# Optimization experiments

Hardware: AMD Instinct MI355X
Metric: run time of the kernel (lower is better)

The kernel has to match this reference:

```python
import jax, jax.numpy as jnp
import numpy as np

EMBED = 768
GH = 4        # heads per group
GD = 256      # group dim = GH * head_dim
NSTEPS = 3    # n_pde_steps
DT = 0.05
HJ_H = 0.05   # Heimburg-Jackson dispersion coefficient


def _sh(u, k):
    # shift field content along sequence axis (axis=1) by k with zero boundary
    if k == 0:
        return u
    z = jnp.zeros_like(u)
    if k > 0:
        return z.at[:, k:, :].set(u[:, :-k, :])
    return z.at[:, :k, :].set(u[:, -k:, :])


def _d1(u):
    return 0.5 * (_sh(u, -1) - _sh(u, 1))


def _d2(u):
    return _sh(u, -1) - 2.0 * u + _sh(u, 1)


def _d3(u):
    return 0.5 * (_sh(u, -2) - 2.0 * _sh(u, -1) + 2.0 * _sh(u, 1) - _sh(u, 2))


def _d4(u):
    return _sh(u, -2) - 4.0 * _sh(u, -1) + 6.0 * u - 4.0 * _sh(u, 1) + _sh(u, 2)


def _attn(x, qkv_w, qkv_b, ow, ob, nh):
    # standard causal multi-head attention on one head group
    B, T, D = x.shape
    hd = D // nh
    qkv = x @ qkv_w + qkv_b                      # (B,T,3D)
    q, k, v = jnp.split(qkv, 3, axis=-1)
    heads = lambda a: a.reshape(B, T, nh, hd).transpose(0, 2, 1, 3)
    q, k, v = heads(q), heads(k), heads(v)
    s = jnp.einsum('bhqd,bhkd->bhqk', q, k) * (1.0 / np.sqrt(hd))
    causal = jnp.tril(jnp.ones((T, T), dtype=bool))
    s = jnp.where(causal, s, jnp.asarray(-1e9, s.dtype))
    p = jax.nn.softmax(s, axis=-1)
    o = jnp.einsum('bhqk,bhkd->bhqd', p, v).transpose(0, 2, 1, 3).reshape(B, T, D)
    return o @ ow + ob


def _sine_gordon(u):
    # u_tt = u_xx - sin(u), semi-implicit Euler (leapfrog-like)
    w = jnp.zeros_like(u)
    for _ in range(NSTEPS):
        w = w + DT * (_d2(u) - jnp.sin(u))
        u = u + DT * w
    return u


def _kdv(u):
    # u_t = -6 u u_x - u_xxx, explicit Euler
    for _ in range(NSTEPS):
        u = u + DT * (-6.0 * u * _d1(u) - _d3(u))
    return u


def _hj(u):
    # Heimburg-Jackson: u_tt = d_xx((c0^2 + p u + q u^2) u) - h u_xxxx
    # with c0=1, p=-1, q=1
    w = jnp.zeros_like(u)
    for _ in range(NSTEPS):
        f = u - u * u + u * u * u
        w = w + DT * (_d2(f) - HJ_H * _d4(u))
        u = u + DT * w
    return u


def setup_inputs() -> dict:
    key = jax.random.key(0)
    ks = jax.random.split(key, 16)
    s = 0.02
    d, gd = EMBED, GD
    inp = {'x': jax.random.normal(ks[0], (4, 2048, d), dtype=jnp.float32)}
    inp['in_w'] = jax.random.normal(ks[1], (d, d), jnp.float32) * s
    inp['in_b'] = jnp.zeros((d,), jnp.float32)
    for i, n in enumerate(['sg', 'kdv', 'hj']):
        inp[n + '_qkv_w'] = jax.random.normal(ks[2 + 4 * i], (gd, 3 * gd), jnp.float32) * s
        inp[n + '_qkv_b'] = jnp.zeros((3 * gd,), jnp.float32)
        inp[n + '_out_w'] = jax.random.normal(ks[3 + 4 * i], (gd, gd), jnp.float32) * s
        inp[n + '_out_b'] = jnp.zeros((gd,), jnp.float32)
    inp['out_w'] = jax.random.normal(ks[14], (d, d), jnp.float32) * s
    inp['out_b'] = jnp.zeros((d,), jnp.float32)
    return inp


def reference(x, in_w, in_b,
              sg_qkv_w, sg_qkv_b, sg_out_w, sg_out_b,
              kdv_qkv_w, kdv_qkv_b, kdv_out_w, kdv_out_b,
              hj_qkv_w, hj_qkv_b, hj_out_w, hj_out_b,
              out_w, out_b):
    h = x @ in_w + in_b
    xg = jnp.split(h, [GD, 2 * GD], axis=-1)
    sg = _sine_gordon(_attn(xg[0], sg_qkv_w, sg_qkv_b, sg_out_w, sg_out_b, GH))
    kv = _kdv(_attn(xg[1], kdv_qkv_w, kdv_qkv_b, kdv_out_w, kdv_out_b, GH))
    hj = _hj(_attn(xg[2], hj_qkv_w, hj_qkv_b, hj_out_w, hj_out_b, GH))
    out = jnp.concatenate([sg, kv, hj], axis=-1)
    return out @ out_w + out_b
```

## Files before the change

### kernel.cpp

```cpp
#include <hip/hip_runtime.h>
#include <math.h>

#define B_   4
#define T_   2048
#define D_   768
#define M_   8192
#define GD_  256
#define NH_  4
#define HD_  64

typedef short  s16x8 __attribute__((ext_vector_type(8)));
typedef __bf16 bfx8  __attribute__((ext_vector_type(8)));
typedef float  fx4   __attribute__((ext_vector_type(4)));

#define LOG2E 1.44269504088896f
#define QSCALE (0.125f * LOG2E)

__device__ __forceinline__ short f2bf(float f) {
  union { float f; unsigned u; } v; v.f = f;
  unsigned r = v.u + 0x7fffu + ((v.u >> 16) & 1u);
  return (short)(r >> 16);
}

__device__ __forceinline__ unsigned cvt_pk_bf16(float lo, float hi) {
  unsigned r;
  asm("v_cvt_pk_bf16_f32 %0, %1, %2" : "=v"(r) : "v"(lo), "v"(hi));
  return r;
}

struct PW { const short* p0; const short* p1; const short* p2; };
struct PB { const float* p0; const float* p1; const float* p2; };
__device__ __forceinline__ const short* selw(const PW& s, int z) {
  return z == 0 ? s.p0 : (z == 1 ? s.p1 : s.p2);
}
__device__ __forceinline__ const float* selb(const PB& s, int z) {
  return z == 0 ? s.p0 : (z == 1 ? s.p1 : s.p2);
}

template<int AT, int OBF, int MODE>
__global__ __launch_bounds__(256) void gemm_mfma(
    const void* __restrict__ Avoid, long sA, int lda,
    PW Wp, PB Bp, int K,
    void* __restrict__ C, long sC, int ldc,
    void* __restrict__ xtra)
{
  __shared__ short As[128 * 72];
  __shared__ short Bs[64 * 72];

  const int z = blockIdx.z;
  const short* Ab16 = (const short*)Avoid + (long)z * sA;
  const float* Ab32 = (const float*)Avoid + (long)z * sA;
  const short* Wb = selw(Wp, z);
  const float* bb = selb(Bp, z);

  const int n0 = blockIdx.x * 64;
  const int m0 = blockIdx.y * 128;
  const int tid = threadIdx.x, lane = tid & 63, w = tid >> 6;
  const int wm = w >> 1, wn = w & 1;
  const int quad = lane >> 4, mr = lane & 15;

  const int r0 = tid >> 3;
  const int cs = (tid & 7) * 8;

  fx4 acc[4][2] = {};
  s16x8 ar[4], br[2];

  auto loadA = [&](int k0) {
#pragma unroll
    for (int gg = 0; gg < 4; ++gg) {
      if (AT) {
        const float* p = Ab32 + (long)(m0 + r0 + 32 * gg) * lda + k0 + cs;
        float4 f0 = *(const float4*)p;
        float4 f1 = *(const float4*)(p + 4);
        short o[8] = { f2bf(f0.x), f2bf(f0.y), f2bf(f0.z), f2bf(f0.w),
                       f2bf(f1.x), f2bf(f1.y), f2bf(f1.z), f2bf(f1.w) };
        ar[gg] = *(s16x8*)o;
      } else {
        ar[gg] = *(const s16x8*)(Ab16 + (long)(m0 + r0 + 32 * gg) * lda + k0 + cs);
      }
    }
  };
  auto loadB = [&](int k0) {
#pragma unroll
    for (int hh = 0; hh < 2; ++hh)
      br[hh] = *(const s16x8*)(Wb + (long)(n0 + r0 + 32 * hh) * K + k0 + cs);
  };

  loadA(0); loadB(0);

  for (int k0 = 0; k0 < K; k0 += 64) {
#pragma unroll
    for (int gg = 0; gg < 4; ++gg)
      *(s16x8*)&As[(r0 + 32 * gg) * 72 + cs] = ar[gg];
#pragma unroll
    for (int hh = 0; hh < 2; ++hh)
      *(s16x8*)&Bs[(r0 + 32 * hh) * 72 + cs] = br[hh];
    __syncthreads();

    if (k0 + 64 < K) { loadA(k0 + 64); loadB(k0 + 64); }

#pragma unroll
    for (int ks = 0; ks < 2; ++ks) {
      bfx8 af[4], bf[2];
#pragma unroll
      for (int i = 0; i < 4; ++i)
        af[i] = *(const bfx8*)&As[(wm * 64 + i * 16 + mr) * 72 + ks * 32 + quad * 8];
#pragma unroll
      for (int j = 0; j < 2; ++j)
        bf[j] = *(const bfx8*)&Bs[(wn * 32 + j * 16 + mr) * 72 + ks * 32 + quad * 8];
#pragma unroll
      for (int i = 0; i < 4; ++i)
#pragma unroll
        for (int j = 0; j < 2; ++j)
          acc[i][j] = __builtin_amdgcn_mfma_f32_16x16x32_bf16(af[i], bf[j], acc[i][j], 0, 0, 0);
    }
    __syncthreads();
  }

  float* Cf = (float*)C + (long)z * sC;
  short* Cs = (short*)C + (long)z * sC;
#pragma unroll
  for (int j = 0; j < 2; ++j) {
    const int col = n0 + wn * 32 + j * 16 + mr;
    const float bvx = bb[col];
#pragma unroll
    for (int i = 0; i < 4; ++i) {
      const int row0 = m0 + wm * 64 + i * 16 + quad * 4;
      if (MODE == 2) {
        const int rb = row0 >> 11, t0 = row0 & 2047;
        fx4 o;
#pragma unroll
        for (int r = 0; r < 4; ++r) o[r] = acc[i][j][r] + bvx;
        *(fx4*)((float*)xtra + (((long)z * B_ + rb) * GD_ + col) * T_ + t0) = o;
      } else if (MODE == 1 && col >= 512) {
        const int h = (col - 512) >> 6, hd = (col - 512) & 63;
        const int rb = row0 >> 11, t0 = row0 & 2047;
        short o4[4];
#pragma unroll
        for (int r = 0; r < 4; ++r) o4[r] = f2bf(acc[i][j][r] + bvx);
        *(short4*)((short*)xtra + ((((long)z * B_ + rb) * NH_ + h) * HD_ + hd) * T_ + t0) =
            *(short4*)o4;
      } else {
        const float sc = (MODE == 1 && col < 256) ? QSCALE : 1.0f;
#pragma unroll
        for (int r = 0; r < 4; ++r) {
          float v = (acc[i][j][r] + bvx) * sc;
          if (OBF) Cs[(long)(row0 + r) * ldc + col] = f2bf(v);
          else     Cf[(long)(row0 + r) * ldc + col] = v;
        }
      }
    }
  }
}

__global__ __launch_bounds__(256) void flash_attn_mfma(
    short* __restrict__ qkv, const short* __restrict__ vtb)
{
  __shared__ short Ks[64][72];
  __shared__ short Vs[80][72];
  __shared__ short Ps[128 * 64];

  const int bid = blockIdx.x;
  const int Q = 15 - (bid / 48);
  const int combo = bid % 48;
  const int g = combo % 3, bh = combo / 3;
  const int b = bh >> 2, h = bh & 3;

  short* base = qkv + ((size_t)g * M_ + (size_t)b * T_) * D_;
  short*       Qp = base + h * HD_;
  const short* Kp = base + GD_ + h * HD_;
  const short* Vtp = vtb + ((((size_t)g * B_ + b) * NH_ + h) * HD_) * T_;

  const int tid = threadIdx.x, lane = tid & 63, w = tid >> 6;
  const int quad = lane >> 4, mr = lane & 15;
  const int q0 = Q * 128, wr = w * 32;
  const int qhi = q0 + wr + 31;

  const int sra = tid >> 3, sc = (tid & 7) * 8;

  if (tid < 128) {
    const short ov = 0x3F80;
    s16x8 one = { ov, ov, ov, ov, ov, ov, ov, ov };
    *(s16x8*)&Vs[64 + (tid >> 3)][(tid & 7) * 8] = one;
  }

  bfx8 aq[2][2];
#pragma unroll
  for (int f = 0; f < 2; ++f)
#pragma unroll
    for (int ks = 0; ks < 2; ++ks)
      aq[f][ks] = *(const bfx8*)(Qp + (size_t)(q0 + wr + f * 16 + mr) * D_ +
                                 ks * 32 + quad * 8);

  s16x8 kreg0 = *(const s16x8*)(Kp + (size_t)sra * D_ + sc);
  s16x8 kreg1 = *(const s16x8*)(Kp + (size_t)(sra + 32) * D_ + sc);
  s16x8 vreg0 = *(const s16x8*)(Vtp + (size_t)sra * T_ + sc);
  s16x8 vreg1 = *(const s16x8*)(Vtp + (size_t)(sra + 32) * T_ + sc);

  fx4 Oa[2][5] = {};

  char* PsB = (char*)&Ps[0];
  const int rot = (mr & 7) << 4;

  const int ktmax = 2 * Q + 1;
  for (int kt = 0; kt <= ktmax; ++kt) {
    *(s16x8*)&Ks[sra][sc]      = kreg0;
    *(s16x8*)&Ks[sra + 32][sc] = kreg1;
    *(s16x8*)&Vs[sra][sc]      = vreg0;
    *(s16x8*)&Vs[sra + 32][sc] = vreg1;
    __syncthreads();

    if (kt < ktmax) {
      const int kn = (kt + 1) * 64;
      kreg0 = *(const s16x8*)(Kp + (size_t)(kn + sra) * D_ + sc);
      kreg1 = *(const s16x8*)(Kp + (size_t)(kn + sra + 32) * D_ + sc);
      vreg0 = *(const s16x8*)(Vtp + (size_t)sra * T_ + kn + sc);
      vreg1 = *(const s16x8*)(Vtp + (size_t)(sra + 32) * T_ + kn + sc);
    }

    if (kt * 64 <= qhi) {
      fx4 st[4][2] = {};
#pragma unroll
      for (int ks = 0; ks < 2; ++ks) {
        bfx8 bk[4];
#pragma unroll
        for (int jj = 0; jj < 4; ++jj)
          bk[jj] = *(const bfx8*)&Ks[jj * 16 + mr][ks * 32 + quad * 8];
#pragma unroll
        for (int jj = 0; jj < 4; ++jj)
#pragma unroll
          for (int f = 0; f < 2; ++f)
            st[jj][f] = __builtin_amdgcn_mfma_f32_16x16x32_bf16(bk[jj], aq[f][ks], st[jj][f], 0, 0, 0);
      }

      if (kt >= 2 * Q) {
#pragma unroll
        for (int jj = 0; jj < 4; ++jj)
#pragma unroll
          for (int f = 0; f < 2; ++f) {
            const int qg = q0 + wr + f * 16 + mr;
            const int kvg0 = kt * 64 + jj * 16 + quad * 4;
#pragma unroll
            for (int r = 0; r < 4; ++r)
              if (kvg0 + r > qg) st[jj][f][r] = -1e30f;
          }
      }

#pragma unroll
      for (int f = 0; f < 2; ++f) {
        const int rowb = (wr + f * 16 + mr) << 7;
#pragma unroll
        for (int jj = 0; jj < 4; ++jj) {
          float e0 = exp2f(st[jj][f][0]);
          float e1 = exp2f(st[jj][f][1]);
          float e2 = exp2f(st[jj][f][2]);
          float e3 = exp2f(st[jj][f][3]);
          unsigned pk0 = cvt_pk_bf16(e0, e1);
          unsigned pk1 = cvt_pk_bf16(e2, e3);
          unsigned long long pv = (unsigned long long)pk0 |
                                  ((unsigned long long)pk1 << 32);
          const int kb = (jj * 32 + quad * 8) ^ rot;
          *(unsigned long long*)(PsB + rowb + kb) = pv;
        }
      }

#pragma unroll
      for (int ks = 0; ks < 2; ++ks) {
        bfx8 ap[2];
#pragma unroll
        for (int f = 0; f < 2; ++f) {
          const int rowb = (wr + f * 16 + mr) << 7;
          const int kb = (ks * 64 + quad * 16) ^ rot;
          ap[f] = *(const bfx8*)(PsB + rowb + kb);
        }
#pragma unroll
        for (int j = 0; j < 5; ++j) {
          bfx8 bv = *(const bfx8*)&Vs[j * 16 + mr][ks * 32 + quad * 8];
#pragma unroll
          for (int f = 0; f < 2; ++f)
            Oa[f][j] = __builtin_amdgcn_mfma_f32_16x16x32_bf16(ap[f], bv, Oa[f][j], 0, 0, 0);
        }
      }
    }
    __syncthreads();
  }

#pragma unroll
  for (int f = 0; f < 2; ++f)
#pragma unroll
    for (int r = 0; r < 4; ++r) {
      const float inv = 1.0f / Oa[f][4][r];
      const int row = q0 + wr + f * 16 + quad * 4 + r;
#pragma unroll
      for (int j = 0; j < 4; ++j)
        Qp[(size_t)row * D_ + j * 16 + mr] = f2bf(Oa[f][j][r] * inv);
    }
}

__device__ __forceinline__ float fhj(float x) { return x - x * x + x * x * x; }

__global__ __launch_bounds__(256) void pde_kernel(
    const float* __restrict__ ut, short* __restrict__ ub)
{
  __shared__ short ob[4][2056];

  const int cg = blockIdx.x, b = blockIdx.y, g = blockIdx.z;
  const int tid = threadIdx.x;
  const int c = tid >> 6, lane = tid & 63;
  const int t0 = lane * 32;
  const float dt = 0.05f;

  const float* src = ut + (((size_t)g * B_ + b) * GD_ + cg * 4 + c) * T_ + t0;

  float uc[36];
#pragma unroll
  for (int q = 0; q < 8; ++q)
    *(fx4*)&uc[2 + q * 4] = *(const fx4*)(src + q * 4);

  {
    float h0 = __shfl_up(uc[32], 1);
    float h1 = __shfl_up(uc[33], 1);
    float h2 = __shfl_down(uc[2], 1);
    float h3 = __shfl_down(uc[3], 1);
    uc[0]  = (lane == 0)  ? 0.f : h0;
    uc[1]  = (lane == 0)  ? 0.f : h1;
    uc[34] = (lane == 63) ? 0.f : h2;
    uc[35] = (lane == 63) ? 0.f : h3;
  }

  float wreg[32];
#pragma unroll
  for (int i = 0; i < 32; ++i) wreg[i] = 0.f;

  for (int step = 0; step < 3; ++step) {
    float nu[32];
#pragma unroll
    for (int tt = 0; tt < 32; ++tt) {
      float um2 = uc[tt], um1 = uc[tt + 1], u = uc[tt + 2];
      float up1 = uc[tt + 3], up2 = uc[tt + 4];
      if (g == 0) {
        float d2 = up1 - 2.f * u + um1;
        wreg[tt] += dt * (d2 - __sinf(u));
        nu[tt] = u + dt * wreg[tt];
      } else if (g == 1) {
        float d1 = 0.5f * (up1 - um1);
        float d3 = 0.5f * (up2 - 2.f * up1 + 2.f * um1 - um2);
        nu[tt] = u + dt * (-6.f * u * d1 - d3);
      } else {
        float d2f = fhj(up1) - 2.f * fhj(u) + fhj(um1);
        float d4  = up2 - 4.f * up1 + 6.f * u - 4.f * um1 + um2;
        wreg[tt] += dt * (d2f - 0.05f * d4);
        nu[tt] = u + dt * wreg[tt];
      }
    }
    float h0 = __shfl_up(nu[30], 1);
    float h1 = __shfl_up(nu[31], 1);
    float h2 = __shfl_down(nu[0], 1);
    float h3 = __shfl_down(nu[1], 1);
    uc[0]  = (lane == 0)  ? 0.f : h0;
    uc[1]  = (lane == 0)  ? 0.f : h1;
    uc[34] = (lane == 63) ? 0.f : h2;
    uc[35] = (lane == 63) ? 0.f : h3;
#pragma unroll
    for (int i = 0; i < 32; ++i) uc[2 + i] = nu[i];
  }

  short o16[32];
#pragma unroll
  for (int i = 0; i < 32; ++i) o16[i] = f2bf(uc[2 + i]);
#pragma unroll
  for (int q = 0; q < 4; ++q)
    *(s16x8*)&ob[c][t0 + q * 8] = *(s16x8*)&o16[q * 8];
  __syncthreads();

  short* dst = ub + (size_t)b * T_ * D_ + g * GD_ + cg * 4;
#pragma unroll
  for (int q = 0; q < 8; ++q) {
    int t = tid + q * 256;
    short o4[4];
#pragma unroll
    for (int cc = 0; cc < 4; ++cc) o4[cc] = ob[cc][t];
    *(short4*)(dst + (size_t)t * D_) = *(short4*)o4;
  }
}

struct PrepArgs {
  const float* w[8]; short* wt[8];
  int K[8], N[8];
  int tend[8];
};

__global__ __launch_bounds__(256) void prep_kernel(PrepArgs pa)
{
  const int bid = blockIdx.x, tid = threadIdx.x;
  __shared__ float Ws[32][33];
  int ti = 0;
#pragma unroll
  for (int i = 0; i < 8; ++i) if (bid >= pa.tend[i]) ti = i + 1;
  const int tloc = bid - (ti ? pa.tend[ti - 1] : 0);
  const int K = pa.K[ti], N = pa.N[ti];
  const int ntx = N >> 5;
  const int k0 = (tloc / ntx) * 32, n0 = (tloc % ntx) * 32;
  const float* W = pa.w[ti];
  short* WT = pa.wt[ti];
  const int tx = tid & 31, ty = tid >> 5;

#pragma unroll
  for (int i = 0; i < 4; ++i)
    Ws[ty + 8 * i][tx] = W[(long)(k0 + ty + 8 * i) * N + n0 + tx];
  __syncthreads();
#pragma unroll
  for (int i = 0; i < 4; ++i) {
    int r = ty + 8 * i;
    WT[(long)(n0 + r) * K + k0 + tx] = f2bf(Ws[tx][r]);
  }
}

extern "C" void kernel_launch(void* const* d_in, const int* in_sizes, int n_in,
                              void* d_out, int out_size, void* d_ws, size_t ws_size,
                              hipStream_t stream)
{
  (void)in_sizes; (void)n_in; (void)out_size; (void)ws_size;

  const float* x         = (const float*)d_in[0];
  const float* in_w      = (const float*)d_in[1];
  const float* in_b      = (const float*)d_in[2];
  const float* sg_qkv_w  = (const float*)d_in[3];
  const float* sg_qkv_b  = (const float*)d_in[4];
  const float* sg_out_w  = (const float*)d_in[5];
  const float* sg_out_b  = (const float*)d_in[6];
  const float* kdv_qkv_w = (const float*)d_in[7];
  const float* kdv_qkv_b = (const float*)d_in[8];
  const float* kdv_out_w = (const float*)d_in[9];
  const float* kdv_out_b = (const float*)d_in[10];
  const float* hj_qkv_w  = (const float*)d_in[11];
  const float* hj_qkv_b  = (const float*)d_in[12];
  const float* hj_out_w  = (const float*)d_in[13];
  const float* hj_out_b  = (const float*)d_in[14];
  const float* out_w     = (const float*)d_in[15];
  const float* out_b     = (const float*)d_in[16];
  float* out = (float*)d_out;

  const size_t MD = (size_t)M_ * D_;
  short* base = (short*)d_ws;
  short* hb   = base + MD;
  float* uf   = (float*)d_ws;
  short* qkvb = base + 2 * MD;
  short* ub16 = qkvb + 3 * MD;
  short* wts  = ub16 + MD;
  short* in_wT  = wts;
  short* qkvT0  = in_wT + 589824;
  short* qkvT1  = qkvT0 + 196608;
  short* qkvT2  = qkvT1 + 196608;
  short* outT0  = qkvT2 + 196608;
  short* outT1  = outT0 + 65536;
  short* outT2  = outT1 + 65536;
  short* out_wT = outT2 + 65536;
  short* vtb    = out_wT + 589824;

  dim3 blk(256);

  PrepArgs pa;
  const float* wsrc[8] = { in_w, sg_qkv_w, kdv_qkv_w, hj_qkv_w,
                           sg_out_w, kdv_out_w, hj_out_w, out_w };
  short* wdst[8] = { in_wT, qkvT0, qkvT1, qkvT2, outT0, outT1, outT2, out_wT };
  int Ksz[8] = { 768, 256, 256, 256, 256, 256, 256, 768 };
  int Nsz[8] = { 768, 768, 768, 768, 256, 256, 256, 768 };
  int cum = 0;
  for (int i = 0; i < 8; ++i) {
    pa.w[i] = wsrc[i]; pa.wt[i] = wdst[i]; pa.K[i] = Ksz[i]; pa.N[i] = Nsz[i];
    cum += (Ksz[i] >> 5) * (Nsz[i] >> 5);
    pa.tend[i] = cum;
  }
  prep_kernel<<<dim3((unsigned)cum), blk, 0, stream>>>(pa);

  gemm_mfma<1, 1, 0><<<dim3(12, 64, 1), blk, 0, stream>>>(
      x, 0, D_, PW{in_wT, in_wT, in_wT}, PB{in_b, in_b, in_b}, D_,
      hb, 0, D_, nullptr);

  gemm_mfma<0, 1, 1><<<dim3(12, 64, 3), blk, 0, stream>>>(
      hb, 256, D_,
      PW{qkvT0, qkvT1, qkvT2}, PB{sg_qkv_b, kdv_qkv_b, hj_qkv_b}, GD_,
      qkvb, (long)MD, D_, vtb);

  flash_attn_mfma<<<dim3(768), blk, 0, stream>>>(qkvb, vtb);

  gemm_mfma<0, 0, 2><<<dim3(4, 64, 3), blk, 0, stream>>>(
      qkvb, (long)MD, D_,
      PW{outT0, outT1, outT2}, PB{sg_out_b, kdv_out_b, hj_out_b}, GD_,
      uf, 0, 0, uf);

  pde_kernel<<<dim3(64, 4, 3), blk, 0, stream>>>(uf, ub16);

  gemm_mfma<0, 0, 0><<<dim3(12, 64, 1), blk, 0, stream>>>(
      ub16, 0, D_, PW{out_wT, out_wT, out_wT}, PB{out_b, out_b, out_b}, D_,
      out, 0, D_, nullptr);
}
```

Baseline: 305.9 us.

## Use direct global-to-LDS loads with double buffering and XOR swizzle in GEMM

For the bf16-input GEMM path, register-staged loads are replaced with global_load_lds 16-byte direct-to-LDS transfers into double-buffered shared tiles. A waitcnt/barrier pipeline overlaps the next tile's fetch with MFMA compute on the current one. Padded LDS rows are replaced by an XOR swizzle to avoid bank conflicts, and the fp32-input path also adopts the swizzle. This aims to cut register staging and LDS write latency, but relies on correct vmcnt accounting and doubles the LDS footprint.

New measurement: 307.5 us. Within noise of the previous version (+0.5%).

```diff
diff --git a/kernel.cpp b/kernel.cpp
--- a/kernel.cpp
+++ b/kernel.cpp
@@ -28,6 +28,12 @@
   return r;
 }
 
+__device__ __forceinline__ void gload16(const void* g, void* l) {
+  __builtin_amdgcn_global_load_lds(
+      (const __attribute__((address_space(1))) unsigned int*)g,
+      (__attribute__((address_space(3))) unsigned int*)l, 16, 0, 0);
+}
+
 struct PW { const short* p0; const short* p1; const short* p2; };
 struct PB { const float* p0; const float* p1; const float* p2; };
 __device__ __forceinline__ const short* selw(const PW& s, int z) {
@@ -44,8 +50,8 @@
     void* __restrict__ C, long sC, int ldc,
     void* __restrict__ xtra)
 {
-  __shared__ short As[128 * 72];
-  __shared__ short Bs[64 * 72];
+  __shared__ short As[2][128 * 64];
+  __shared__ short Bs[2][64 * 64];
 
   const int z = blockIdx.z;
   const short* Ab16 = (const short*)Avoid + (long)z * sA;
@@ -59,62 +65,101 @@
   const int wm = w >> 1, wn = w & 1;
   const int quad = lane >> 4, mr = lane & 15;
 
-  const int r0 = tid >> 3;
-  const int cs = (tid & 7) * 8;
-
   fx4 acc[4][2] = {};
-  s16x8 ar[4], br[2];
-
-  auto loadA = [&](int k0) {
-#pragma unroll
-    for (int gg = 0; gg < 4; ++gg) {
-      if (AT) {
+
+  auto compute = [&](const short* Ab, const short* Bb) {
+#pragma unroll
+    for (int ks = 0; ks < 2; ++ks) {
+      const int cc = ks * 32 + quad * 8;
+      const int swz = cc ^ ((mr & 7) * 8);
+      bfx8 af[4], bf[2];
+#pragma unroll
+      for (int i = 0; i < 4; ++i)
+        af[i] = *(const bfx8*)&Ab[(wm * 64 + i * 16 + mr) * 64 + swz];
+#pragma unroll
+      for (int j = 0; j < 2; ++j)
+        bf[j] = *(const bfx8*)&Bb[(wn * 32 + j * 16 + mr) * 64 + swz];
+#pragma unroll
+      for (int i = 0; i < 4; ++i)
+#pragma unroll
+        for (int j = 0; j < 2; ++j)
+          acc[i][j] = __builtin_amdgcn_mfma_f32_16x16x32_bf16(af[i], bf[j], acc[i][j], 0, 0, 0);
+    }
+  };
+
+  if (AT) {
+    const int r0 = tid >> 3;
+    const int cs = (tid & 7) * 8;
+    const int wswz = cs ^ ((r0 & 7) * 8);
+    s16x8 ar[4], br[2];
+
+    auto loadA = [&](int k0) {
+#pragma unroll
+      for (int gg = 0; gg < 4; ++gg) {
         const float* p = Ab32 + (long)(m0 + r0 + 32 * gg) * lda + k0 + cs;
         float4 f0 = *(const float4*)p;
         float4 f1 = *(const float4*)(p + 4);
         short o[8] = { f2bf(f0.x), f2bf(f0.y), f2bf(f0.z), f2bf(f0.w),
                        f2bf(f1.x), f2bf(f1.y), f2bf(f1.z), f2bf(f1.w) };
         ar[gg] = *(s16x8*)o;
+      }
+    };
+    auto loadB = [&](int k0) {
+#pragma unroll
+      for (int hh = 0; hh < 2; ++hh)
+        br[hh] = *(const s16x8*)(Wb + (long)(n0 + r0 + 32 * hh) * K + k0 + cs);
+    };
+
+    loadA(0); loadB(0);
+    for (int k0 = 0; k0 < K; k0 += 64) {
+#pragma unroll
+      for (int gg = 0; gg < 4; ++gg)
+        *(s16x8*)&As[0][(r0 + 32 * gg) * 64 + wswz] = ar[gg];
+#pragma unroll
+      for (int hh = 0; hh < 2; ++hh)
+        *(s16x8*)&Bs[0][(r0 + 32 * hh) * 64 + wswz] = br[hh];
+      __syncthreads();
+      if (k0 + 64 < K) { loadA(k0 + 64); loadB(k0 + 64); }
+      compute(&As[0][0], &Bs[0][0]);
+      __syncthreads();
+    }
+  } else {
+    const int lrow = lane >> 3, lcol = lane & 7;
+
+    auto stageA = [&](short* dst, int k0) {
+#pragma unroll
+      for (int i = 0; i < 4; ++i) {
+        const int r = i * 32 + w * 8 + lrow;
+        const int swz = (lcol * 8) ^ ((r & 7) * 8);
+        gload16(Ab16 + (long)(m0 + r) * lda + k0 + swz,
+                dst + (i * 32 + w * 8) * 64);
+      }
+    };
+    auto stageB = [&](short* dst, int k0) {
+#pragma unroll
+      for (int i = 0; i < 2; ++i) {
+        const int r = i * 32 + w * 8 + lrow;
+        const int swz = (lcol * 8) ^ ((r & 7) * 8);
+        gload16(Wb + (long)(n0 + r) * K + k0 + swz,
+                dst + (i * 32 + w * 8) * 64);
+      }
+    };
+
+    stageA(&As[0][0], 0); stageB(&Bs[0][0], 0);
+    const int NT = K >> 6;
+    for (int t = 0; t < NT; ++t) {
+      const int cur = t & 1;
+      if (t + 1 < NT) {
+        stageA(&As[cur ^ 1][0], (t + 1) * 64);
+        stageB(&Bs[cur ^ 1][0], (t + 1) * 64);
+        asm volatile("s_waitcnt vmcnt(6)" ::: "memory");
       } else {
-        ar[gg] = *(const s16x8*)(Ab16 + (long)(m0 + r0 + 32 * gg) * lda + k0 + cs);
-      }
-    }
-  };
-  auto loadB = [&](int k0) {
-#pragma unroll
-    for (int hh = 0; hh < 2; ++hh)
-      br[hh] = *(const s16x8*)(Wb + (long)(n0 + r0 + 32 * hh) * K + k0 + cs);
-  };
-
-  loadA(0); loadB(0);
-
-  for (int k0 = 0; k0 < K; k0 += 64) {
-#pragma unroll
-    for (int gg = 0; gg < 4; ++gg)
-      *(s16x8*)&As[(r0 + 32 * gg) * 72 + cs] = ar[gg];
-#pragma unroll
-    for (int hh = 0; hh < 2; ++hh)
-      *(s16x8*)&Bs[(r0 + 32 * hh) * 72 + cs] = br[hh];
-    __syncthreads();
-
-    if (k0 + 64 < K) { loadA(k0 + 64); loadB(k0 + 64); }
-
-#pragma unroll
-    for (int ks = 0; ks < 2; ++ks) {
-      bfx8 af[4], bf[2];
-#pragma unroll
-      for (int i = 0; i < 4; ++i)
-        af[i] = *(const bfx8*)&As[(wm * 64 + i * 16 + mr) * 72 + ks * 32 + quad * 8];
-#pragma unroll
-      for (int j = 0; j < 2; ++j)
-        bf[j] = *(const bfx8*)&Bs[(wn * 32 + j * 16 + mr) * 72 + ks * 32 + quad * 8];
-#pragma unroll
-      for (int i = 0; i < 4; ++i)
-#pragma unroll
-        for (int j = 0; j < 2; ++j)
-          acc[i][j] = __builtin_amdgcn_mfma_f32_16x16x32_bf16(af[i], bf[j], acc[i][j], 0, 0, 0);
-    }
-    __syncthreads();
+        asm volatile("s_waitcnt vmcnt(0)" ::: "memory");
+      }
+      __builtin_amdgcn_s_barrier();
+      compute(&As[cur][0], &Bs[cur][0]);
+      __builtin_amdgcn_s_barrier();
+    }
   }
 
   float* Cf = (float*)C + (long)z * sC;
```
